# Kernel tuning notes

Measured on AMD Instinct MI355X. Metric: run time of the kernel, lower is better.

## Reference

```python
import jax, jax.numpy as jnp
import numpy as np

ALPHA = 0.2  # LeakyReLU negative slope


def setup_inputs() -> dict:
    key = jax.random.key(0)
    k1, k2, k3 = jax.random.split(key, 3)
    B, N, F_IN, F_OUT = 8, 2048, 128, 64
    h = jax.random.normal(k1, (B, N, F_IN), dtype=jnp.float32)
    # nn.Linear(in, out, bias=False).weight is [out, in]; we store the transposed
    # matmul-ready form W: [F_IN, F_OUT].
    W = jax.random.normal(k2, (F_IN, F_OUT), dtype=jnp.float32) * 0.05
    # attn_fc: Linear(2*F_OUT, 1, bias=False) -> weight vector a: [2*F_OUT]
    a = jax.random.normal(k3, (2 * F_OUT,), dtype=jnp.float32) * 0.05
    return {"h": h, "W": W, "a": a}


def reference(h, W, a):
    # h: [B, N, F_in], W: [F_in, F_out], a: [2*F_out]
    F_out = W.shape[1]
    Wh = h @ W  # [B, N, F_out]
    # cat([Wh_i, Wh_j]) @ a == Wh_i @ a1 + Wh_j @ a2 -- identical math,
    # avoids materializing the [B, N, N, 2F] tensor.
    s_i = Wh @ a[:F_out]  # [B, N] contribution of row node i
    s_j = Wh @ a[F_out:]  # [B, N] contribution of col node j
    e = jax.nn.leaky_relu(s_i[:, :, None] + s_j[:, None, :], negative_slope=ALPHA)  # [B, N, N]
    attn = jax.nn.softmax(e, axis=-1)  # softmax over neighbors j
    h_prime = jnp.einsum('bij,bjf->bif', attn, Wh)  # [B, N, F_out]
    return h_prime.mean(axis=1)  # [B, F_out]
```

## Files before the change

### kernel.cpp

```cpp
#include <hip/hip_runtime.h>
#include <hip/hip_bf16.h>


#define B 8
#define N 2048
#define BN (B * N)
#define FIN 128
#define FOUT 64
#define ALPHA 0.2f
#define JS 32
#define SJ (N / JS)

__global__ __launch_bounds__(256) void k2_uv(const float* __restrict__ h,
                                             const float* __restrict__ W,
                                             const float* __restrict__ a,
                                             float* __restrict__ u, float* __restrict__ v,
                                             float* __restrict__ out) {
    __shared__ float sa[2 * FOUT];
    __shared__ float sw[2 * FIN];
    int t = threadIdx.x, bid = blockIdx.x;
    if (bid == 0) {
        out[t] = 0.f;
        out[t + 256] = 0.f;
    }
    if (t < 2 * FOUT) sa[t] = a[t];
    __syncthreads();
    {
        int kk = t >> 4, f0 = (t & 15) * 4;
        float a1x = sa[f0], a1y = sa[f0 + 1], a1z = sa[f0 + 2], a1w = sa[f0 + 3];
        float a2x = sa[FOUT + f0], a2y = sa[FOUT + f0 + 1], a2z = sa[FOUT + f0 + 2], a2w = sa[FOUT + f0 + 3];
        #pragma unroll
        for (int p = 0; p < 8; ++p) {
            int k = p * 16 + kk;
            float4 w4 = *(const float4*)(W + k * FOUT + f0);
            float p1 = w4.x * a1x + w4.y * a1y + w4.z * a1z + w4.w * a1w;
            float p2 = w4.x * a2x + w4.y * a2y + w4.z * a2z + w4.w * a2w;
            #pragma unroll
            for (int o = 1; o < 16; o <<= 1) {
                p1 += __shfl_xor(p1, o);
                p2 += __shfl_xor(p2, o);
            }
            if ((t & 15) == 0) { sw[k] = p1; sw[FIN + k] = p2; }
        }
    }
    __syncthreads();
    int wave = t >> 6, lane = t & 63;
    const float2 w1x = *(const float2*)(sw + lane * 2);
    const float2 w2x = *(const float2*)(sw + FIN + lane * 2);
    int node0 = bid * 32 + wave * 8;
    #pragma unroll
    for (int it = 0; it < 8; ++it) {
        int node = node0 + it;
        const float2 hx = *(const float2*)(h + (size_t)node * FIN + lane * 2);
        float p1 = hx.x * w1x.x + hx.y * w1x.y;
        float p2 = hx.x * w2x.x + hx.y * w2x.y;
        #pragma unroll
        for (int o = 32; o; o >>= 1) {
            p1 += __shfl_xor(p1, o);
            p2 += __shfl_xor(p2, o);
        }
        if (lane == 0) { u[node] = p1; v[node] = p2; }
    }
}

__global__ __launch_bounds__(256) void k3_pass1(const float* __restrict__ u,
                                                const float* __restrict__ v,
                                                float* __restrict__ Ap, float* __restrict__ Bp) {
    __shared__ float sv[SJ], se[SJ], sf[SJ];
    int bid = blockIdx.x;
    int b = bid >> 6, ic = (bid >> 5) & 1, js = bid & 31;
    int t = threadIdx.x;
    if (t < SJ) {
        float vj = v[b * N + js * SJ + t];
        sv[t] = vj;
        se[t] = expf(vj);
        sf[t] = expf(ALPHA * vj);
    }
    __syncthreads();
    float th[4], A[4], Bm[4];
    #pragma unroll
    for (int r = 0; r < 4; ++r) {
        th[r] = -u[b * N + ic * 1024 + r * 256 + t];
        A[r] = 0.f; Bm[r] = 0.f;
    }
    for (int j = 0; j < SJ; j += 4) {
        float4 vv = *(const float4*)&sv[j];
        float4 ee = *(const float4*)&se[j];
        float4 ff = *(const float4*)&sf[j];
        #pragma unroll
        for (int r = 0; r < 4; ++r) {
            A[r] += (vv.x > th[r]) ? ee.x : 0.f;  Bm[r] += (vv.x > th[r]) ? 0.f : ff.x;
            A[r] += (vv.y > th[r]) ? ee.y : 0.f;  Bm[r] += (vv.y > th[r]) ? 0.f : ff.y;
            A[r] += (vv.z > th[r]) ? ee.z : 0.f;  Bm[r] += (vv.z > th[r]) ? 0.f : ff.z;
            A[r] += (vv.w > th[r]) ? ee.w : 0.f;  Bm[r] += (vv.w > th[r]) ? 0.f : ff.w;
        }
    }
    #pragma unroll
    for (int r = 0; r < 4; ++r) {
        int i = ic * 1024 + r * 256 + t;
        Ap[js * BN + b * N + i] = A[r];
        Bp[js * BN + b * N + i] = Bm[r];
    }
}

__global__ __launch_bounds__(256) void k4_pass2(const float* __restrict__ u,
                                                const float* __restrict__ v,
                                                const float* __restrict__ Ap,
                                                const float* __restrict__ Bp,
                                                float* __restrict__ cp) {
    __shared__ float spA[256], spB[256];
    __shared__ float su[64], sr1[64], sr2[64];
    int bid = blockIdx.x;
    int b = bid >> 6, jc = (bid >> 5) & 1, is = bid & 31;
    int t = threadIdx.x;
    {
        int lane = t & 63, ch = t >> 6;
        int ii0 = b * N + is * 64 + lane;
        float pA = 0.f, pB = 0.f;
        #pragma unroll
        for (int s2 = 0; s2 < 8; ++s2) {
            int s = ch * 8 + s2;
            pA += Ap[s * BN + ii0];
            pB += Bp[s * BN + ii0];
        }
        spA[ch * 64 + lane] = pA;
        spB[ch * 64 + lane] = pB;
    }
    __syncthreads();
    if (t < 64) {
        float As = (spA[t] + spA[64 + t]) + (spA[128 + t] + spA[192 + t]);
        float Bs = (spB[t] + spB[64 + t]) + (spB[128 + t] + spB[192 + t]);
        float ui = u[b * N + is * 64 + t];
        float eu = expf(ui);
        float fu = expf(ALPHA * ui);
        float inv = 1.0f / (eu * As + fu * Bs);
        su[t] = ui; sr1[t] = eu * inv; sr2[t] = fu * inv;
    }
    __syncthreads();
    float vj[4], th[4], Cn[4], Dn[4];
    #pragma unroll
    for (int r = 0; r < 4; ++r) {
        vj[r] = v[b * N + jc * 1024 + r * 256 + t];
        th[r] = -vj[r];
        Cn[r] = 0.f; Dn[r] = 0.f;
    }
    for (int i = 0; i < 64; i += 4) {
        float4 uu = *(const float4*)&su[i];
        float4 r1 = *(const float4*)&sr1[i];
        float4 r2 = *(const float4*)&sr2[i];
        #pragma unroll
        for (int r = 0; r < 4; ++r) {
            Cn[r] += (uu.x > th[r]) ? r1.x : 0.f;  Dn[r] += (uu.x > th[r]) ? 0.f : r2.x;
            Cn[r] += (uu.y > th[r]) ? r1.y : 0.f;  Dn[r] += (uu.y > th[r]) ? 0.f : r2.y;
            Cn[r] += (uu.z > th[r]) ? r1.z : 0.f;  Dn[r] += (uu.z > th[r]) ? 0.f : r2.z;
            Cn[r] += (uu.w > th[r]) ? r1.w : 0.f;  Dn[r] += (uu.w > th[r]) ? 0.f : r2.w;
        }
    }
    #pragma unroll
    for (int r = 0; r < 4; ++r) {
        int j = jc * 1024 + r * 256 + t;
        cp[is * BN + b * N + j] = expf(vj[r]) * Cn[r] + expf(ALPHA * vj[r]) * Dn[r];
    }
}

__global__ __launch_bounds__(256) void k5_out(const float* __restrict__ h,
                                              const float* __restrict__ W,
                                              const float* __restrict__ cp,
                                              float* __restrict__ out) {
    __shared__ float scp[256];
    __shared__ float sc[32];
    __shared__ float sg2[256];
    __shared__ float sg[128];
    __shared__ float so[256];
    int b = blockIdx.x >> 6, ns = blockIdx.x & 63;
    int t = threadIdx.x;
    {
        int n = t & 31, ch = t >> 5;
        int nn = b * N + ns * 32 + n;
        float c = 0.f;
        #pragma unroll
        for (int s2 = 0; s2 < 4; ++s2) c += cp[(ch * 4 + s2) * BN + nn];
        scp[ch * 32 + n] = c;
    }
    __syncthreads();
    if (t < 32) {
        float c = 0.f;
        #pragma unroll
        for (int ch = 0; ch < 8; ++ch) c += scp[ch * 32 + t];
        sc[t] = c;
    }
    __syncthreads();
    {
        int k = t & 127, half = t >> 7;
        float a0 = 0.f, a1 = 0.f;
        int base = b * N + ns * 32 + half * 16;
        #pragma unroll
        for (int n = 0; n < 16; n += 2) {
            a0 += sc[half * 16 + n]     * h[(size_t)(base + n)     * FIN + k];
            a1 += sc[half * 16 + n + 1] * h[(size_t)(base + n + 1) * FIN + k];
        }
        sg2[half * 128 + k] = a0 + a1;
    }
    __syncthreads();
    if (t < 128) sg[t] = sg2[t] + sg2[128 + t];
    __syncthreads();
    {
        int f = t & 63, q = t >> 6;
        float acc = 0.f;
        #pragma unroll
        for (int kk2 = 0; kk2 < 32; ++kk2) {
            int kk = q * 32 + kk2;
            acc += sg[kk] * W[kk * FOUT + f];
        }
        so[q * 64 + f] = acc;
    }
    __syncthreads();
    if (t < 64) {
        float r = ((so[t] + so[64 + t]) + (so[128 + t] + so[192 + t])) * (1.0f / (float)N);
        atomicAdd(out + b * FOUT + t, r);
    }
}

extern "C" void kernel_launch(void* const* d_in, const int* in_sizes, int n_in,
                              void* d_out, int out_size, void* d_ws, size_t ws_size,
                              hipStream_t stream) {
    const float* h = (const float*)d_in[0];
    const float* W = (const float*)d_in[1];
    const float* a = (const float*)d_in[2];
    float* out = (float*)d_out;

    float* ws = (float*)d_ws;
    float* u  = ws;
    float* v  = u + BN;
    float* Ap = v + BN;
    float* Bp = Ap + JS * BN;
    float* cp = Bp + JS * BN;

    k2_uv<<<512, 256, 0, stream>>>(h, W, a, u, v, out);
    k3_pass1<<<512, 256, 0, stream>>>(u, v, Ap, Bp);
    k4_pass2<<<512, 256, 0, stream>>>(u, v, Ap, Bp, cp);
    k5_out<<<512, 256, 0, stream>>>(h, W, cp, out);
}
```

Before: 86.81 us.

## Double j-split count with full-row blocks and vectorize u/v projection

```diff
diff --git a/kernel.cpp b/kernel.cpp
--- a/kernel.cpp
+++ b/kernel.cpp
@@ -8,8 +8,12 @@
 #define FIN 128
 #define FOUT 64
 #define ALPHA 0.2f
-#define JS 32
+#define JS 64
 #define SJ (N / JS)
+
+__device__ __forceinline__ float dot4(float4 x, float4 y) {
+    return x.x * y.x + x.y * y.y + x.z * y.z + x.w * y.w;
+}
 
 __global__ __launch_bounds__(256) void k2_uv(const float* __restrict__ h,
                                              const float* __restrict__ W,
@@ -26,40 +30,38 @@
     if (t < 2 * FOUT) sa[t] = a[t];
     __syncthreads();
     {
-        int kk = t >> 4, f0 = (t & 15) * 4;
-        float a1x = sa[f0], a1y = sa[f0 + 1], a1z = sa[f0 + 2], a1w = sa[f0 + 3];
-        float a2x = sa[FOUT + f0], a2y = sa[FOUT + f0 + 1], a2z = sa[FOUT + f0 + 2], a2w = sa[FOUT + f0 + 3];
-        #pragma unroll
-        for (int p = 0; p < 8; ++p) {
-            int k = p * 16 + kk;
-            float4 w4 = *(const float4*)(W + k * FOUT + f0);
-            float p1 = w4.x * a1x + w4.y * a1y + w4.z * a1z + w4.w * a1w;
-            float p2 = w4.x * a2x + w4.y * a2y + w4.z * a2z + w4.w * a2w;
-            #pragma unroll
-            for (int o = 1; o < 16; o <<= 1) {
-                p1 += __shfl_xor(p1, o);
-                p2 += __shfl_xor(p2, o);
-            }
-            if ((t & 15) == 0) { sw[k] = p1; sw[FIN + k] = p2; }
-        }
+        int k = t >> 1, half = t & 1;
+        float p1 = 0.f, p2 = 0.f;
+        #pragma unroll
+        for (int i = 0; i < 8; ++i) {
+            float4 w4 = *(const float4*)(W + k * FOUT + half * 32 + i * 4);
+            float4 a1 = *(const float4*)(sa + half * 32 + i * 4);
+            float4 a2 = *(const float4*)(sa + FOUT + half * 32 + i * 4);
+            p1 += dot4(w4, a1);
+            p2 += dot4(w4, a2);
+        }
+        p1 += __shfl_xor(p1, 1);
+        p2 += __shfl_xor(p2, 1);
+        if (half == 0) { sw[k] = p1; sw[FIN + k] = p2; }
     }
     __syncthreads();
     int wave = t >> 6, lane = t & 63;
-    const float2 w1x = *(const float2*)(sw + lane * 2);
-    const float2 w2x = *(const float2*)(sw + FIN + lane * 2);
+    int hl = lane & 31;
+    const float4 w1x = *(const float4*)(sw + hl * 4);
+    const float4 w2x = *(const float4*)(sw + FIN + hl * 4);
     int node0 = bid * 32 + wave * 8;
     #pragma unroll
-    for (int it = 0; it < 8; ++it) {
-        int node = node0 + it;
-        const float2 hx = *(const float2*)(h + (size_t)node * FIN + lane * 2);
-        float p1 = hx.x * w1x.x + hx.y * w1x.y;
-        float p2 = hx.x * w2x.x + hx.y * w2x.y;
-        #pragma unroll
-        for (int o = 32; o; o >>= 1) {
+    for (int it = 0; it < 4; ++it) {
+        int node = node0 + it * 2 + (lane >> 5);
+        const float4 hx = *(const float4*)(h + (size_t)node * FIN + hl * 4);
+        float p1 = dot4(hx, w1x);
+        float p2 = dot4(hx, w2x);
+        #pragma unroll
+        for (int o = 1; o < 32; o <<= 1) {
             p1 += __shfl_xor(p1, o);
             p2 += __shfl_xor(p2, o);
         }
-        if (lane == 0) { u[node] = p1; v[node] = p2; }
+        if (hl == 0) { u[node] = p1; v[node] = p2; }
     }
 }
 
@@ -68,7 +70,7 @@
                                                 float* __restrict__ Ap, float* __restrict__ Bp) {
     __shared__ float sv[SJ], se[SJ], sf[SJ];
     int bid = blockIdx.x;
-    int b = bid >> 6, ic = (bid >> 5) & 1, js = bid & 31;
+    int b = bid >> 6, js = bid & 63;
     int t = threadIdx.x;
     if (t < SJ) {
         float vj = v[b * N + js * SJ + t];
@@ -77,18 +79,19 @@
         sf[t] = expf(ALPHA * vj);
     }
     __syncthreads();
-    float th[4], A[4], Bm[4];
-    #pragma unroll
-    for (int r = 0; r < 4; ++r) {
-        th[r] = -u[b * N + ic * 1024 + r * 256 + t];
+    float th[8], A[8], Bm[8];
+    #pragma unroll
+    for (int r = 0; r < 8; ++r) {
+        th[r] = -u[b * N + r * 256 + t];
         A[r] = 0.f; Bm[r] = 0.f;
     }
+    #pragma unroll
     for (int j = 0; j < SJ; j += 4) {
         float4 vv = *(const float4*)&sv[j];
         float4 ee = *(const float4*)&se[j];
         float4 ff = *(const float4*)&sf[j];
         #pragma unroll
-        for (int r = 0; r < 4; ++r) {
+        for (int r = 0; r < 8; ++r) {
             A[r] += (vv.x > th[r]) ? ee.x : 0.f;  Bm[r] += (vv.x > th[r]) ? 0.f : ff.x;
             A[r] += (vv.y > th[r]) ? ee.y : 0.f;  Bm[r] += (vv.y > th[r]) ? 0.f : ff.y;
             A[r] += (vv.z > th[r]) ? ee.z : 0.f;  Bm[r] += (vv.z > th[r]) ? 0.f : ff.z;
@@ -96,8 +99,8 @@
         }
     }
     #pragma unroll
-    for (int r = 0; r < 4; ++r) {
-        int i = ic * 1024 + r * 256 + t;
+    for (int r = 0; r < 8; ++r) {
+        int i = r * 256 + t;
         Ap[js * BN + b * N + i] = A[r];
         Bp[js * BN + b * N + i] = Bm[r];
     }
@@ -109,13 +112,13 @@
                                                 const float* __restrict__ Bp,
                                                 float* __restrict__ cp) {
     __shared__ float spA[256], spB[256];
-    __shared__ float su[64], sr1[64], sr2[64];
+    __shared__ float su[SJ], sr1[SJ], sr2[SJ];
     int bid = blockIdx.x;
-    int b = bid >> 6, jc = (bid >> 5) & 1, is = bid & 31;
+    int b = bid >> 6, is = bid & 63;
     int t = threadIdx.x;
     {
-        int lane = t & 63, ch = t >> 6;
-        int ii0 = b * N + is * 64 + lane;
+        int n = t & 31, ch = t >> 5;
+        int ii0 = b * N + is * 32 + n;
         float pA = 0.f, pB = 0.f;
         #pragma unroll
         for (int s2 = 0; s2 < 8; ++s2) {
@@ -123,33 +126,38 @@
             pA += Ap[s * BN + ii0];
             pB += Bp[s * BN + ii0];
         }
-        spA[ch * 64 + lane] = pA;
-        spB[ch * 64 + lane] = pB;
-    }
-    __syncthreads();
-    if (t < 64) {
-        float As = (spA[t] + spA[64 + t]) + (spA[128 + t] + spA[192 + t]);
-        float Bs = (spB[t] + spB[64 + t]) + (spB[128 + t] + spB[192 + t]);
-        float ui = u[b * N + is * 64 + t];
+        spA[ch * 32 + n] = pA;
+        spB[ch * 32 + n] = pB;
+    }
+    __syncthreads();
+    if (t < 32) {
+        float As = 0.f, Bs = 0.f;
+        #pragma unroll
+        for (int ch = 0; ch < 8; ++ch) {
+            As += spA[ch * 32 + t];
+            Bs += spB[ch * 32 + t];
+        }
+        float ui = u[b * N + is * 32 + t];
         float eu = expf(ui);
         float fu = expf(ALPHA * ui);
         float inv = 1.0f / (eu * As + fu * Bs);
         su[t] = ui; sr1[t] = eu * inv; sr2[t] = fu * inv;
     }
     __syncthreads();
-    float vj[4], th[4], Cn[4], Dn[4];
-    #pragma unroll
-    for (int r = 0; r < 4; ++r) {
-        vj[r] = v[b * N + jc * 1024 + r * 256 + t];
+    float vj[8], th[8], Cn[8], Dn[8];
+    #pragma unroll
+    for (int r = 0; r < 8; ++r) {
+        vj[r] = v[b * N + r * 256 + t];
         th[r] = -vj[r];
         Cn[r] = 0.f; Dn[r] = 0.f;
     }
-    for (int i = 0; i < 64; i += 4) {
+    #pragma unroll
+    for (int i = 0; i < SJ; i += 4) {
         float4 uu = *(const float4*)&su[i];
         float4 r1 = *(const float4*)&sr1[i];
         float4 r2 = *(const float4*)&sr2[i];
         #pragma unroll
-        for (int r = 0; r < 4; ++r) {
+        for (int r = 0; r < 8; ++r) {
             Cn[r] += (uu.x > th[r]) ? r1.x : 0.f;  Dn[r] += (uu.x > th[r]) ? 0.f : r2.x;
             Cn[r] += (uu.y > th[r]) ? r1.y : 0.f;  Dn[r] += (uu.y > th[r]) ? 0.f : r2.y;
             Cn[r] += (uu.z > th[r]) ? r1.z : 0.f;  Dn[r] += (uu.z > th[r]) ? 0.f : r2.z;
@@ -157,8 +165,8 @@
         }
     }
     #pragma unroll
-    for (int r = 0; r < 4; ++r) {
-        int j = jc * 1024 + r * 256 + t;
+    for (int r = 0; r < 8; ++r) {
+        int j = r * 256 + t;
         cp[is * BN + b * N + j] = expf(vj[r]) * Cn[r] + expf(ALPHA * vj[r]) * Dn[r];
     }
 }
@@ -179,7 +187,7 @@
         int nn = b * N + ns * 32 + n;
         float c = 0.f;
         #pragma unroll
-        for (int s2 = 0; s2 < 4; ++s2) c += cp[(ch * 4 + s2) * BN + nn];
+        for (int s2 = 0; s2 < 8; ++s2) c += cp[(ch * 8 + s2) * BN + nn];
         scp[ch * 32 + n] = c;
     }
     __syncthreads();
```

Result: faster. 84.63 us, median of 2 (-2.5%).
